# Optimization experiments

Measured on AMD Instinct MI355X. Metric: run time of the kernel, lower is better.

Reference implementation:

```python
import jax, jax.numpy as jnp
import numpy as np

B, N, C = 4, 2048, 768
H = 12
D = C // H  # head_dim = 64
SCALE = D ** -0.5


def setup_inputs() -> dict:
    key = jax.random.key(0)
    ks = jax.random.split(key, 9)
    x = jax.random.normal(ks[0], (B, N, C), dtype=jnp.float32)
    k_in = jax.random.normal(ks[1], (B, N, C), dtype=jnp.float32)
    v_in = jax.random.normal(ks[2], (B, N, C), dtype=jnp.float32)
    rel_pos_bias = jax.random.normal(ks[3], (H, N, N), dtype=jnp.float32)
    # learned params (nn.Linear stores weight [out, in]; y = x @ W.T + b)
    s = C ** -0.5
    Wq = jax.random.normal(ks[4], (C, C), dtype=jnp.float32) * s
    Wk = jax.random.normal(ks[5], (C, C), dtype=jnp.float32) * s
    Wv = jax.random.normal(ks[6], (C, C), dtype=jnp.float32) * s
    Wp = jax.random.normal(ks[7], (C, C), dtype=jnp.float32) * s
    bp = jax.random.normal(ks[8], (C,), dtype=jnp.float32) * 0.01
    return {"x": x, "k_in": k_in, "v_in": v_in, "rel_pos_bias": rel_pos_bias,
            "Wq": Wq, "Wk": Wk, "Wv": Wv, "Wp": Wp, "bp": bp}


def reference(x, k_in, v_in, rel_pos_bias, Wq, Wk, Wv, Wp, bp):
    # linear projections (no q/k/v bias since qkv_bias=False)
    q = jnp.einsum('bnc,dc->bnd', x, Wq)      # [B,N,C]
    k = jnp.einsum('bnc,dc->bnd', k_in, Wk)   # [B,Nk,C]
    v = jnp.einsum('bnc,dc->bnd', v_in, Wv)   # [B,Nv,C]
    # split heads -> [B,H,N,D]
    q = q.reshape(B, N, H, D).transpose(0, 2, 1, 3) * SCALE
    k = k.reshape(B, -1, H, D).transpose(0, 2, 1, 3)
    v = v.reshape(B, -1, H, D).transpose(0, 2, 1, 3)
    attn = jnp.einsum('bhnd,bhmd->bhnm', q, k)          # [B,H,N,Nk]
    attn = attn + rel_pos_bias[None]                    # additive rel-pos bias
    attn = jax.nn.softmax(attn, axis=-1)
    out = jnp.einsum('bhnm,bhmd->bhnd', attn, v)        # [B,H,N,D]
    out = out.transpose(0, 2, 1, 3).reshape(B, N, C)
    return jnp.einsum('bnc,dc->bnd', out, Wp) + bp
```

## Files before the change

kernel.cpp:

```cpp
#include <hip/hip_runtime.h>
#include <stdint.h>
#include <stddef.h>

#define B_ 4
#define N_ 2048
#define C_ 768
#define H_ 12
#define M_ (B_ * N_)

typedef __attribute__((ext_vector_type(8))) short bf16x8_t;
typedef __attribute__((ext_vector_type(4))) float f32x4_t;

__device__ __forceinline__ unsigned pack2_bf16(float f0, float f1) {
  unsigned u0 = __builtin_bit_cast(unsigned, f0) + 0x8000u;
  unsigned u1 = __builtin_bit_cast(unsigned, f1) + 0x8000u;
  return __builtin_amdgcn_perm(u1, u0, 0x07060302u);
}

__device__ __forceinline__ short f2bf(float f) {
  unsigned u = __builtin_bit_cast(unsigned, f);
  u = (u + 0x7FFFu + ((u >> 16) & 1u)) >> 16;
  return (short)u;
}
__device__ __forceinline__ short f2bf_fast(float f) {
  return (short)((__builtin_bit_cast(unsigned, f) + 0x8000u) >> 16);
}

__device__ __forceinline__ void gload_lds16(const short* g, const short* l) {
  __builtin_amdgcn_global_load_lds(
      (const __attribute__((address_space(1))) void*)g,
      (__attribute__((address_space(3))) void*)l, 16, 0, 0);
}

#define XV 1572864
#define WV 147456
__global__ __launch_bounds__(256) void cvt_all(
    const float* __restrict__ x, const float* __restrict__ kin, const float* __restrict__ vin,
    const float* __restrict__ wq, const float* __restrict__ wk, const float* __restrict__ wv,
    const float* __restrict__ wp,
    unsigned short* __restrict__ xb, unsigned short* __restrict__ kb, unsigned short* __restrict__ vb,
    unsigned short* __restrict__ wqb, unsigned short* __restrict__ wkb, unsigned short* __restrict__ wvb,
    unsigned short* __restrict__ wpb)
{
  int i = blockIdx.x * 256 + threadIdx.x;
  const float* s; unsigned short* d; int off;
  if      (i < XV)            { s = x;   d = xb;  off = i; }
  else if (i < 2 * XV)        { s = kin; d = kb;  off = i - XV; }
  else if (i < 3 * XV)        { s = vin; d = vb;  off = i - 2 * XV; }
  else if (i < 3 * XV + WV)   { s = wq;  d = wqb; off = i - 3 * XV; }
  else if (i < 3 * XV + 2*WV) { s = wk;  d = wkb; off = i - 3 * XV - WV; }
  else if (i < 3 * XV + 3*WV) { s = wv;  d = wvb; off = i - 3 * XV - 2 * WV; }
  else                        { s = wp;  d = wpb; off = i - 3 * XV - 3 * WV; }
  float4 v = ((const float4*)s)[off];
  uint2 p;
  p.x = pack2_bf16(v.x, v.y);
  p.y = pack2_bf16(v.z, v.w);
  ((uint2*)d)[off] = p;
}

__global__ __launch_bounds__(256) void proj_qkv(
    const short* __restrict__ xb, const short* __restrict__ kb, const short* __restrict__ vb,
    const short* __restrict__ wqb, const short* __restrict__ wkb, const short* __restrict__ wvb,
    short* __restrict__ q_ws, short* __restrict__ k_ws, short* __restrict__ vt_ws)
{
  const int z = blockIdx.z;
  const short* A = (z == 0) ? xb : (z == 1) ? kb : vb;
  const short* W = (z == 0) ? wqb : (z == 1) ? wkb : wvb;
  const int m0 = blockIdx.x * 128;
  const int n0 = blockIdx.y * 128;

  __shared__ __align__(16) short smem[2 * 16384];

  const int t = threadIdx.x;
  const int w = t >> 6, L = t & 63, L15 = L & 15, quad = L >> 4;
  const int wm = w & 1, wn = w >> 1;

  f32x4_t acc[4][4] = {};

  const short* ga = A + (size_t)(m0 + w * 32 + (L >> 3)) * C_ + (L & 7) * 8;
  const short* gb = W + (size_t)(n0 + w * 32 + (L >> 3)) * C_ + (L & 7) * 8;
  const int lofs = (w * 32) * 64;

  #pragma unroll
  for (int i = 0; i < 4; ++i) {
    gload_lds16(ga + (size_t)i * 8 * C_, smem + lofs + i * 512);
    gload_lds16(gb + (size_t)i * 8 * C_, smem + 8192 + lofs + i * 512);
  }
  __syncthreads();

  for (int T = 0; T < 12; ++T) {
    const int cur = T & 1;
    const short* Acur = smem + cur * 16384;
    const short* Bcur = Acur + 8192;

    if (T < 11) {
      short* Anxt = smem + (cur ^ 1) * 16384;
      const int k1 = (T + 1) * 64;
      #pragma unroll
      for (int i = 0; i < 4; ++i) {
        gload_lds16(ga + (size_t)i * 8 * C_ + k1, Anxt + lofs + i * 512);
        gload_lds16(gb + (size_t)i * 8 * C_ + k1, Anxt + 8192 + lofs + i * 512);
      }
    }

    #pragma unroll
    for (int kk = 0; kk < 2; ++kk) {
      bf16x8_t af[4], bf[4];
      #pragma unroll
      for (int mt = 0; mt < 4; ++mt)
        af[mt] = *(const bf16x8_t*)&Acur[(wm * 64 + mt * 16 + L15) * 64 + kk * 32 + quad * 8];
      #pragma unroll
      for (int nt = 0; nt < 4; ++nt)
        bf[nt] = *(const bf16x8_t*)&Bcur[(wn * 64 + nt * 16 + L15) * 64 + kk * 32 + quad * 8];
      #pragma unroll
      for (int mt = 0; mt < 4; ++mt)
        #pragma unroll
        for (int nt = 0; nt < 4; ++nt)
          acc[mt][nt] = __builtin_amdgcn_mfma_f32_16x16x32_bf16(af[mt], bf[nt], acc[mt][nt], 0, 0, 0);
    }

    __syncthreads();
  }

  if (z != 2) {
    short* outp = (z == 0) ? q_ws : k_ws;
    const float mul = (z == 0) ? 0.125f : 1.0f;
    #pragma unroll
    for (int mt = 0; mt < 4; ++mt) {
      const int m_base = m0 + wm * 64 + mt * 16 + quad * 4;
      #pragma unroll
      for (int nt = 0; nt < 4; ++nt) {
        const int c = n0 + wn * 64 + nt * 16 + L15;
        const int h = c >> 6, d = c & 63;
        #pragma unroll
        for (int r = 0; r < 4; ++r) {
          const int m = m_base + r;
          const int b = m >> 11, n = m & 2047;
          outp[((size_t)(b * H_ + h) * N_ + n) * 64 + d] = f2bf(acc[mt][nt][r] * mul);
        }
      }
    }
  } else {
    #pragma unroll
    for (int mt = 0; mt < 4; ++mt) {
      const int ml = wm * 64 + mt * 16 + quad * 4;
      #pragma unroll
      for (int nt = 0; nt < 4; ++nt) {
        const int cl = wn * 64 + nt * 16 + L15;
        #pragma unroll
        for (int r = 0; r < 4; ++r)
          smem[cl * 136 + ml + r] = f2bf(acc[mt][nt][r]);
      }
    }
    __syncthreads();
    const int bb = m0 >> 11;
    const int nn0 = m0 & 2047;
    #pragma unroll
    for (int pp = 0; pp < 8; ++pp) {
      const int cl = pp * 16 + (t >> 4);
      const int mg = t & 15;
      const uint4 val = *(const uint4*)&smem[cl * 136 + mg * 8];
      const int cg = n0 + cl;
      *(uint4*)&vt_ws[(((size_t)(bb * H_ + (cg >> 6))) * 64 + (cg & 63)) * N_ + nn0 + mg * 8] = val;
    }
  }
}

__global__ __launch_bounds__(256, 3) void attn(
    const short* __restrict__ q_ws, const short* __restrict__ k_ws,
    const short* __restrict__ vt_ws, const float* __restrict__ rpb,
    short* __restrict__ attn_out)
{
  const int p  = blockIdx.x;
  const int lw = (p & 7) * 96 + (p >> 3);
  const int h  = lw >> 6;
  const int xl = lw & 63;
  const int b  = xl & 3;
  const int m0 = (xl >> 2) * 128;
  const int bh = b * H_ + h;

  __shared__ __align__(16) short Ks [2][64 * 64];
  __shared__ __align__(16) short Vts[2][64 * 64];
  __shared__ __align__(16) short Ps [4][32 * 64];

  const int t = threadIdx.x;
  const int w = t >> 6, L = t & 63, L15 = L & 15, quad = L >> 4;

  const short* qp  = q_ws  + ((size_t)bh * N_ + m0) * 64;
  const short* kp  = k_ws  + (size_t)bh * N_ * 64;
  const short* vtp = vt_ws + (size_t)bh * 64 * N_;
  const float* bpb = rpb + (size_t)h * N_ * N_;

  const int srow8 = L >> 3;
  const int scolS = ((L & 7) ^ srow8) * 8;
  const short* gk_base = kp  + (size_t)(w * 16 + srow8) * 64 + scolS;
  const short* gv_base = vtp + (size_t)(w * 16 + srow8) * N_ + scolS;

  bf16x8_t aq[2][2];
  #pragma unroll
  for (int mt = 0; mt < 2; ++mt)
    #pragma unroll
    for (int kk = 0; kk < 2; ++kk)
      aq[mt][kk] = *(const bf16x8_t*)(qp + (size_t)(w * 32 + mt * 16 + L15) * 64 + kk * 32 + quad * 8);

  const float* bq = bpb + (size_t)(m0 + w * 32 + quad * 4) * N_ + L15;

  f32x4_t o[2][4] = {};
  float psum[2][4] = {};
  float bias[2][4][4];

  #pragma unroll
  for (int i = 0; i < 2; ++i) {
    gload_lds16(gk_base + (size_t)i * 8 * 64, &Ks[0][w * 1024 + i * 512]);
    gload_lds16(gv_base + (size_t)i * 8 * N_, &Vts[0][w * 1024 + i * 512]);
  }
  #pragma unroll
  for (int mt = 0; mt < 2; ++mt)
    #pragma unroll
    for (int r = 0; r < 4; ++r)
      #pragma unroll
      for (int nt = 0; nt < 4; ++nt)
        bias[mt][nt][r] = bq[(size_t)(mt * 16 + r) * N_ + nt * 16];
  __syncthreads();

  for (int T = 0; T < 32; ++T) {
    const int cur = T & 1, nxt = cur ^ 1;

    if (T < 31) {
      const int kv1 = (T + 1) * 64;
      #pragma unroll
      for (int i = 0; i < 2; ++i) {
        gload_lds16(gk_base + (size_t)(kv1 + i * 8) * 64, &Ks[nxt][w * 1024 + i * 512]);
        gload_lds16(gv_base + (size_t)i * 8 * N_ + kv1,   &Vts[nxt][w * 1024 + i * 512]);
      }
    }

    f32x4_t s[2][4];
    __builtin_amdgcn_s_setprio(1);
    #pragma unroll
    for (int nt = 0; nt < 4; ++nt) {
      const int row = nt * 16 + L15;
      const char* kbp = (const char*)Ks[cur] + row * 128;
      const int sx = (row & 7) << 4;
      const bf16x8_t b0 = *(const bf16x8_t*)(kbp + ((quad * 16) ^ sx));
      const bf16x8_t b1 = *(const bf16x8_t*)(kbp + ((64 + quad * 16) ^ sx));
      #pragma unroll
      for (int mt = 0; mt < 2; ++mt) {
        f32x4_t sv = {bias[mt][nt][0], bias[mt][nt][1], bias[mt][nt][2], bias[mt][nt][3]};
        sv = __builtin_amdgcn_mfma_f32_16x16x32_bf16(aq[mt][0], b0, sv, 0, 0, 0);
        s[mt][nt] = __builtin_amdgcn_mfma_f32_16x16x32_bf16(aq[mt][1], b1, sv, 0, 0, 0);
      }
    }
    __builtin_amdgcn_s_setprio(0);

    if (T < 31) {
      const float* bqn = bq + (size_t)(T + 1) * 64;
      #pragma unroll
      for (int mt = 0; mt < 2; ++mt)
        #pragma unroll
        for (int r = 0; r < 4; ++r)
          #pragma unroll
          for (int nt = 0; nt < 4; ++nt)
            bias[mt][nt][r] = bqn[(size_t)(mt * 16 + r) * N_ + nt * 16];
    }

    #pragma unroll
    for (int mt = 0; mt < 2; ++mt)
      #pragma unroll
      for (int nt = 0; nt < 4; ++nt)
        #pragma unroll
        for (int r = 0; r < 4; ++r) {
          const float e = __expf(s[mt][nt][r]);
          psum[mt][r] += e;
          const int qrow = mt * 16 + quad * 4 + r;
          const int cb = (nt * 32 + L15 * 2) ^ ((qrow & 7) << 4);
          *(short*)((char*)Ps[w] + qrow * 128 + cb) = f2bf_fast(e);
        }

    __builtin_amdgcn_s_setprio(1);
    #pragma unroll
    for (int kk = 0; kk < 2; ++kk) {
      bf16x8_t pa[2];
      #pragma unroll
      for (int mt = 0; mt < 2; ++mt) {
        const int row = mt * 16 + L15;
        pa[mt] = *(const bf16x8_t*)((char*)Ps[w] + row * 128 +
                                    ((kk * 64 + quad * 16) ^ ((row & 7) << 4)));
      }
      #pragma unroll
      for (int nt = 0; nt < 4; ++nt) {
        const int row = nt * 16 + L15;
        const bf16x8_t vbf = *(const bf16x8_t*)((char*)Vts[cur] + row * 128 +
                                                ((kk * 64 + quad * 16) ^ ((row & 7) << 4)));
        #pragma unroll
        for (int mt = 0; mt < 2; ++mt)
          o[mt][nt] = __builtin_amdgcn_mfma_f32_16x16x32_bf16(pa[mt], vbf, o[mt][nt], 0, 0, 0);
      }
    }
    __builtin_amdgcn_s_setprio(0);

    __syncthreads();
  }

  #pragma unroll
  for (int mt = 0; mt < 2; ++mt)
    #pragma unroll
    for (int r = 0; r < 4; ++r) {
      float v = psum[mt][r];
      v += __shfl_xor(v, 1);
      v += __shfl_xor(v, 2);
      v += __shfl_xor(v, 4);
      v += __shfl_xor(v, 8);
      psum[mt][r] = 1.0f / v;
    }

  #pragma unroll
  for (int mt = 0; mt < 2; ++mt) {
    const int n_base = m0 + w * 32 + mt * 16 + quad * 4;
    #pragma unroll
    for (int nt = 0; nt < 4; ++nt)
      #pragma unroll
      for (int r = 0; r < 4; ++r) {
        const float v = o[mt][nt][r] * psum[mt][r];
        attn_out[((size_t)(b * N_ + n_base + r)) * C_ + h * 64 + nt * 16 + L15] = f2bf(v);
      }
  }
}

__global__ __launch_bounds__(256) void proj_out(
    const short* __restrict__ Abf, const short* __restrict__ wpb,
    const float* __restrict__ bpv, float* __restrict__ out)
{
  const int m0 = blockIdx.x * 128;
  const int n0 = blockIdx.y * 128;

  __shared__ __align__(16) short smem[2 * 16384];

  const int t = threadIdx.x;
  const int w = t >> 6, L = t & 63, L15 = L & 15, quad = L >> 4;
  const int wm = w & 1, wn = w >> 1;

  f32x4_t acc[4][4] = {};

  const short* ga = Abf + (size_t)(m0 + w * 32 + (L >> 3)) * C_ + (L & 7) * 8;
  const short* gb = wpb + (size_t)(n0 + w * 32 + (L >> 3)) * C_ + (L & 7) * 8;
  const int lofs = (w * 32) * 64;

  #pragma unroll
  for (int i = 0; i < 4; ++i) {
    gload_lds16(ga + (size_t)i * 8 * C_, smem + lofs + i * 512);
    gload_lds16(gb + (size_t)i * 8 * C_, smem + 8192 + lofs + i * 512);
  }
  __syncthreads();

  for (int T = 0; T < 12; ++T) {
    const int cur = T & 1;
    const short* Acur = smem + cur * 16384;
    const short* Bcur = Acur + 8192;

    if (T < 11) {
      short* Anxt = smem + (cur ^ 1) * 16384;
      const int k1 = (T + 1) * 64;
      #pragma unroll
      for (int i = 0; i < 4; ++i) {
        gload_lds16(ga + (size_t)i * 8 * C_ + k1, Anxt + lofs + i * 512);
        gload_lds16(gb + (size_t)i * 8 * C_ + k1, Anxt + 8192 + lofs + i * 512);
      }
    }

    #pragma unroll
    for (int kk = 0; kk < 2; ++kk) {
      bf16x8_t af[4], bf[4];
      #pragma unroll
      for (int mt = 0; mt < 4; ++mt)
        af[mt] = *(const bf16x8_t*)&Acur[(wm * 64 + mt * 16 + L15) * 64 + kk * 32 + quad * 8];
      #pragma unroll
      for (int nt = 0; nt < 4; ++nt)
        bf[nt] = *(const bf16x8_t*)&Bcur[(wn * 64 + nt * 16 + L15) * 64 + kk * 32 + quad * 8];
      #pragma unroll
      for (int mt = 0; mt < 4; ++mt)
        #pragma unroll
        for (int nt = 0; nt < 4; ++nt)
          acc[mt][nt] = __builtin_amdgcn_mfma_f32_16x16x32_bf16(af[mt], bf[nt], acc[mt][nt], 0, 0, 0);
    }

    __syncthreads();
  }

  #pragma unroll
  for (int mt = 0; mt < 4; ++mt) {
    const int m_base = m0 + wm * 64 + mt * 16 + quad * 4;
    #pragma unroll
    for (int nt = 0; nt < 4; ++nt) {
      const int c = n0 + wn * 64 + nt * 16 + L15;
      const float bb = bpv[c];
      #pragma unroll
      for (int r = 0; r < 4; ++r)
        out[(size_t)(m_base + r) * C_ + c] = acc[mt][nt][r] + bb;
    }
  }
}

extern "C" void kernel_launch(void* const* d_in, const int* in_sizes, int n_in,
                              void* d_out, int out_size, void* d_ws, size_t ws_size,
                              hipStream_t stream) {
  const float* x    = (const float*)d_in[0];
  const float* k_in = (const float*)d_in[1];
  const float* v_in = (const float*)d_in[2];
  const float* rpb  = (const float*)d_in[3];
  const float* Wq   = (const float*)d_in[4];
  const float* Wk   = (const float*)d_in[5];
  const float* Wv   = (const float*)d_in[6];
  const float* Wp   = (const float*)d_in[7];
  const float* bp   = (const float*)d_in[8];
  float* out = (float*)d_out;

  const size_t SZ = (size_t)B_ * H_ * N_ * 64 * sizeof(short);
  const size_t WSZ = (size_t)C_ * C_ * sizeof(short);
  char* ws = (char*)d_ws;
  short* q_ws  = (short*)(ws);
  short* k_ws  = (short*)(ws + SZ);
  short* vt_ws = (short*)(ws + 2 * SZ);
  short* ao_ws = (short*)(ws + 3 * SZ);
  short* xb    = (short*)(ws + 4 * SZ);
  short* kb    = (short*)(ws + 5 * SZ);
  short* vb    = (short*)(ws + 6 * SZ);
  short* wqb   = (short*)(ws + 7 * SZ);
  short* wkb   = (short*)(ws + 7 * SZ + WSZ);
  short* wvb   = (short*)(ws + 7 * SZ + 2 * WSZ);
  short* wpb   = (short*)(ws + 7 * SZ + 3 * WSZ);

  cvt_all<<<(3 * XV + 4 * WV + 255) / 256, 256, 0, stream>>>(
      x, k_in, v_in, Wq, Wk, Wv, Wp,
      (unsigned short*)xb, (unsigned short*)kb, (unsigned short*)vb,
      (unsigned short*)wqb, (unsigned short*)wkb, (unsigned short*)wvb, (unsigned short*)wpb);
  proj_qkv<<<dim3(M_ / 128, C_ / 128, 3), 256, 0, stream>>>(
      xb, kb, vb, wqb, wkb, wvb, q_ws, k_ws, vt_ws);
  attn<<<dim3(B_ * (N_ / 128) * H_), 256, 0, stream>>>(q_ws, k_ws, vt_ws, rpb, ao_ws);
  proj_out<<<dim3(M_ / 128, C_ / 128), 256, 0, stream>>>(ao_ws, wpb, bp, out);
}
```

Measured before the change: 457.0 us.

## Compute transposed QK^T scores and pass P to PV MFMA via lane shuffles

Swaps the operand order of the QK^T MFMA so each lane holds scores along the key dimension, which lets the bias load as one float4 per tile instead of scalar gathers. The exponentiated probabilities are packed to bf16 pairs and rearranged into the PV MFMA A-operand layout with cross-lane shuffles, removing the per-wave LDS staging buffer and its scalar stores and reads. Row sums are reduced across quads and redistributed with shuffles at the end. This cuts LDS traffic and shared memory use, but adds shuffle instructions and select logic in the inner loop, and it relies on the lane permutation being exactly right.

```diff
diff --git a/kernel.cpp b/kernel.cpp
--- a/kernel.cpp
+++ b/kernel.cpp
@@ -21,9 +21,6 @@
   unsigned u = __builtin_bit_cast(unsigned, f);
   u = (u + 0x7FFFu + ((u >> 16) & 1u)) >> 16;
   return (short)u;
-}
-__device__ __forceinline__ short f2bf_fast(float f) {
-  return (short)((__builtin_bit_cast(unsigned, f) + 0x8000u) >> 16);
 }
 
 __device__ __forceinline__ void gload_lds16(const short* g, const short* l) {
@@ -181,7 +178,6 @@
 
   __shared__ __align__(16) short Ks [2][64 * 64];
   __shared__ __align__(16) short Vts[2][64 * 64];
-  __shared__ __align__(16) short Ps [4][32 * 64];
 
   const int t = threadIdx.x;
   const int w = t >> 6, L = t & 63, L15 = L & 15, quad = L >> 4;
@@ -203,11 +199,15 @@
     for (int kk = 0; kk < 2; ++kk)
       aq[mt][kk] = *(const bf16x8_t*)(qp + (size_t)(w * 32 + mt * 16 + L15) * 64 + kk * 32 + quad * 8);
 
-  const float* bq = bpb + (size_t)(m0 + w * 32 + quad * 4) * N_ + L15;
+  const float* bq = bpb + (size_t)(m0 + w * 32 + L15) * N_ + quad * 4;
 
   f32x4_t o[2][4] = {};
-  float psum[2][4] = {};
-  float bias[2][4][4];
+  float psum[2] = {0.0f, 0.0f};
+  f32x4_t bias[2][4];
+
+  const int sqA = ((quad & 1) << 1) | (quad >> 1);
+  const int srcA = L15 + (sqA << 4);
+  const int srcB = srcA ^ 16;
 
   #pragma unroll
   for (int i = 0; i < 2; ++i) {
@@ -217,10 +217,8 @@
   #pragma unroll
   for (int mt = 0; mt < 2; ++mt)
     #pragma unroll
-    for (int r = 0; r < 4; ++r)
-      #pragma unroll
-      for (int nt = 0; nt < 4; ++nt)
-        bias[mt][nt][r] = bq[(size_t)(mt * 16 + r) * N_ + nt * 16];
+    for (int nt = 0; nt < 4; ++nt)
+      bias[mt][nt] = *(const f32x4_t*)(bq + (size_t)mt * 16 * N_ + nt * 16);
   __syncthreads();
 
   for (int T = 0; T < 32; ++T) {
@@ -242,13 +240,13 @@
       const int row = nt * 16 + L15;
       const char* kbp = (const char*)Ks[cur] + row * 128;
       const int sx = (row & 7) << 4;
-      const bf16x8_t b0 = *(const bf16x8_t*)(kbp + ((quad * 16) ^ sx));
-      const bf16x8_t b1 = *(const bf16x8_t*)(kbp + ((64 + quad * 16) ^ sx));
+      const bf16x8_t k0 = *(const bf16x8_t*)(kbp + ((quad * 16) ^ sx));
+      const bf16x8_t k1 = *(const bf16x8_t*)(kbp + ((64 + quad * 16) ^ sx));
       #pragma unroll
       for (int mt = 0; mt < 2; ++mt) {
-        f32x4_t sv = {bias[mt][nt][0], bias[mt][nt][1], bias[mt][nt][2], bias[mt][nt][3]};
-        sv = __builtin_amdgcn_mfma_f32_16x16x32_bf16(aq[mt][0], b0, sv, 0, 0, 0);
-        s[mt][nt] = __builtin_amdgcn_mfma_f32_16x16x32_bf16(aq[mt][1], b1, sv, 0, 0, 0);
+        f32x4_t sv = bias[mt][nt];
+        sv = __builtin_amdgcn_mfma_f32_16x16x32_bf16(k0, aq[mt][0], sv, 0, 0, 0);
+        s[mt][nt] = __builtin_amdgcn_mfma_f32_16x16x32_bf16(k1, aq[mt][1], sv, 0, 0, 0);
       }
     }
     __builtin_amdgcn_s_setprio(0);
@@ -258,24 +256,23 @@
       #pragma unroll
       for (int mt = 0; mt < 2; ++mt)
         #pragma unroll
-        for (int r = 0; r < 4; ++r)
-          #pragma unroll
-          for (int nt = 0; nt < 4; ++nt)
-            bias[mt][nt][r] = bqn[(size_t)(mt * 16 + r) * N_ + nt * 16];
-    }
-
+        for (int nt = 0; nt < 4; ++nt)
+          bias[mt][nt] = *(const f32x4_t*)(bqn + (size_t)mt * 16 * N_ + nt * 16);
+    }
+
+    unsigned pkv[2][4][2];
     #pragma unroll
     for (int mt = 0; mt < 2; ++mt)
       #pragma unroll
-      for (int nt = 0; nt < 4; ++nt)
-        #pragma unroll
-        for (int r = 0; r < 4; ++r) {
-          const float e = __expf(s[mt][nt][r]);
-          psum[mt][r] += e;
-          const int qrow = mt * 16 + quad * 4 + r;
-          const int cb = (nt * 32 + L15 * 2) ^ ((qrow & 7) << 4);
-          *(short*)((char*)Ps[w] + qrow * 128 + cb) = f2bf_fast(e);
-        }
+      for (int nt = 0; nt < 4; ++nt) {
+        const float e0 = __expf(s[mt][nt][0]);
+        const float e1 = __expf(s[mt][nt][1]);
+        const float e2 = __expf(s[mt][nt][2]);
+        const float e3 = __expf(s[mt][nt][3]);
+        psum[mt] += (e0 + e1) + (e2 + e3);
+        pkv[mt][nt][0] = pack2_bf16(e0, e1);
+        pkv[mt][nt][1] = pack2_bf16(e2, e3);
+      }
 
     __builtin_amdgcn_s_setprio(1);
     #pragma unroll
@@ -283,9 +280,20 @@
       bf16x8_t pa[2];
       #pragma unroll
       for (int mt = 0; mt < 2; ++mt) {
-        const int row = mt * 16 + L15;
-        pa[mt] = *(const bf16x8_t*)((char*)Ps[w] + row * 128 +
-                                    ((kk * 64 + quad * 16) ^ ((row & 7) << 4)));
+        const unsigned sA0 = (quad & 1) ? pkv[mt][2 * kk + 1][0] : pkv[mt][2 * kk][0];
+        const unsigned sA1 = (quad & 1) ? pkv[mt][2 * kk + 1][1] : pkv[mt][2 * kk][1];
+        const unsigned sB0 = (quad & 1) ? pkv[mt][2 * kk][0]     : pkv[mt][2 * kk + 1][0];
+        const unsigned sB1 = (quad & 1) ? pkv[mt][2 * kk][1]     : pkv[mt][2 * kk + 1][1];
+        const unsigned A0 = (unsigned)__shfl((int)sA0, srcA, 64);
+        const unsigned A1 = (unsigned)__shfl((int)sA1, srcA, 64);
+        const unsigned B0 = (unsigned)__shfl((int)sB0, srcB, 64);
+        const unsigned B1 = (unsigned)__shfl((int)sB1, srcB, 64);
+        uint4 fw;
+        fw.x = (quad < 2) ? A0 : B0;
+        fw.y = (quad < 2) ? A1 : B1;
+        fw.z = (quad < 2) ? B0 : A0;
+        fw.w = (quad < 2) ? B1 : A1;
+        pa[mt] = __builtin_bit_cast(bf16x8_t, fw);
       }
       #pragma unroll
       for (int nt = 0; nt < 4; ++nt) {
@@ -302,26 +310,27 @@
     __syncthreads();
   }
 
-  #pragma unroll
-  for (int mt = 0; mt < 2; ++mt)
-    #pragma unroll
-    for (int r = 0; r < 4; ++r) {
-      float v = psum[mt][r];
-      v += __shfl_xor(v, 1);
-      v += __shfl_xor(v, 2);
-      v += __shfl_xor(v, 4);
-      v += __shfl_xor(v, 8);
-      psum[mt][r] = 1.0f / v;
-    }
+  float inv[2];
+  #pragma unroll
+  for (int mt = 0; mt < 2; ++mt) {
+    float v = psum[mt];
+    v += __shfl_xor(v, 16);
+    v += __shfl_xor(v, 32);
+    inv[mt] = v;
+  }
 
   #pragma unroll
   for (int mt = 0; mt < 2; ++mt) {
     const int n_base = m0 + w * 32 + mt * 16 + quad * 4;
+    float rl[4];
+    #pragma unroll
+    for (int r = 0; r < 4; ++r)
+      rl[r] = 1.0f / __shfl(inv[mt], quad * 4 + r);
     #pragma unroll
     for (int nt = 0; nt < 4; ++nt)
       #pragma unroll
       for (int r = 0; r < 4; ++r) {
-        const float v = o[mt][nt][r] * psum[mt][r];
+        const float v = o[mt][nt][r] * rl[r];
         attn_out[((size_t)(b * N_ + n_base + r)) * C_ + h * 64 + nt * 16 + L15] = f2bf(v);
       }
   }
```

Measured after the change: 475.2 us. +4.0%, slower.
